# Performance work log

Hardware: AMD Instinct MI355X
Metric: run time of the kernel (lower is better)

Reference implementation:

```python
import jax, jax.numpy as jnp
import numpy as np

DIM_HEAD = 32  # from init_kwargs; scale = dim_head**-0.5 per the Triton kernel


def setup_inputs() -> dict:
    key = jax.random.key(0)
    k1, k2 = jax.random.split(key)
    B, N, dim = 16, 8192, 128
    D = 4 * DIM_HEAD  # heads * dim_head
    x = jax.random.normal(k1, (B, N, dim), dtype=jnp.float32)
    # ParameterList of 16 stages, each Parameter is randn(2, dim, D) * 0.02
    qk_weights = jax.random.normal(k2, (16, 2, dim, D), dtype=jnp.float32) * 0.02
    return {"x": x, "qk_weights": qk_weights}


def reference(x, qk_weights):
    """FFT-inspired butterfly attention.

    At stage s (stride = 2**s), positions are grouped into blocks of 2*stride;
    the first `stride` elements of each block are 'a', the next `stride` are
    their butterfly partners 'b' (b = a + stride). Q/K are projected from the
    ORIGINAL x with per-stage weights; v is the running value buffer (init x).
    For each pair, a 2-way softmax over [qa.ka, qa.kb] mixes (va, vb).
    """
    B, N, dim = x.shape
    logN = int(round(np.log2(N)))
    D = qk_weights.shape[-1]
    scale = DIM_HEAD ** -0.5

    v = x
    for s in range(logN):
        stride = 1 << s
        Wq = qk_weights[s, 0]  # (dim, D)
        Wk = qk_weights[s, 1]
        q = jnp.einsum('bnd,de->bne', x, Wq) * scale  # (B,N,D)
        k = jnp.einsum('bnd,de->bne', x, Wk)
        G = N // (2 * stride)
        qr = q.reshape(B, G, 2, stride, D)
        kr = k.reshape(B, G, 2, stride, D)
        vr = v.reshape(B, G, 2, stride, dim)
        qa = qr[:, :, 0]
        ka, kb = kr[:, :, 0], kr[:, :, 1]
        va, vb = vr[:, :, 0], vr[:, :, 1]
        s_aa = jnp.sum(qa * ka, axis=-1)  # (B,G,stride)
        s_ab = jnp.sum(qa * kb, axis=-1)
        attn = jax.nn.softmax(jnp.stack([s_aa, s_ab], axis=-1), axis=-1)
        w0 = attn[..., 0:1]
        w1 = attn[..., 1:2]
        out_a = w0 * va + w1 * vb
        out_b = w1 * va + w0 * vb
        v = jnp.stack([out_a, out_b], axis=2).reshape(B, N, dim)
    return v
```

## Files before the change

### kernel.cpp

```cpp
#include <hip/hip_runtime.h>
#include <hip/hip_bf16.h>


typedef __bf16 bf16x8 __attribute__((ext_vector_type(8)));
typedef float  f32x4  __attribute__((ext_vector_type(4)));

#define XSTR 136
#define XB_BYTES  (128 * XSTR * 2)
#define PREP_LDS  (2 * XB_BYTES)
#define LDS_W2    XB_BYTES

#define XW 128
#define LDS_W4    (128 * XW * 2)

#define LDS_MIX   (128 * 128 * 4)

#define WS_DWT_OFF (512 * 1024)
#define DWT4_BYTES (13 * 1024 * 4 * 64 * 4)
#define WS_NEED4   (WS_DWT_OFF + DWT4_BYTES)

__device__ __forceinline__ float ubits(unsigned int u) {
    union { unsigned int u; float f; } v; v.u = u; return v.f;
}
__device__ __forceinline__ unsigned short f2bf(float f) {
    union { float f; unsigned int u; } v; v.f = f;
    unsigned int u = v.u;
    return (unsigned short)((u + 0x7fffu + ((u >> 16) & 1u)) >> 16);
}
__device__ __forceinline__ int swzr(int r) { return ((r >> 1) ^ (r >> 2)) & 15; }

#define DPP_MOV_F(x, ctrl) \
    __int_as_float(__builtin_amdgcn_update_dpp(0, __float_as_int(x), (ctrl), 0xF, 0xF, true))

__device__ __forceinline__ float xlane_u(float x, int u, int lane) {
    if (u == 0) return DPP_MOV_F(x, 0xB1);
    if (u == 1) return DPP_MOV_F(x, 0x4E);
    if (u == 2) return __int_as_float(__builtin_amdgcn_ds_swizzle(__float_as_int(x), 0x101F));
    if (u == 3) return __int_as_float(__builtin_amdgcn_ds_swizzle(__float_as_int(x), 0x201F));
    if (u == 4) return __int_as_float(__builtin_amdgcn_ds_swizzle(__float_as_int(x), 0x401F));
    return __int_as_float(__builtin_amdgcn_ds_bpermute((lane ^ 32) << 2, __float_as_int(x)));
}

__global__ __launch_bounds__(512)
void prep_kernel(const float* __restrict__ qkw, unsigned short* __restrict__ PT) {
    extern __shared__ char smem[];
    unsigned short* wkb = (unsigned short*)smem;
    unsigned short* wqb = (unsigned short*)(smem + XB_BYTES);
    const int s = blockIdx.x;
    const float* Wq = qkw + (size_t)s * 32768;
    const float* Wk = Wq + 16384;
    const int tid = threadIdx.x;
    const int rl = tid >> 5, c4 = tid & 31;
#pragma unroll
    for (int j = 0; j < 8; ++j) {
        int r = j * 16 + rl;
        float4 vq = ((const float4*)Wq)[r * 32 + c4];
        float4 vk = ((const float4*)Wk)[r * 32 + c4];
        ushort4 uq; uq.x = f2bf(vq.x); uq.y = f2bf(vq.y); uq.z = f2bf(vq.z); uq.w = f2bf(vq.w);
        ushort4 uk; uk.x = f2bf(vk.x); uk.y = f2bf(vk.y); uk.z = f2bf(vk.z); uk.w = f2bf(vk.w);
        *(ushort4*)(wqb + r * XSTR + c4 * 4) = uq;
        *(ushort4*)(wkb + r * XSTR + c4 * 4) = uk;
    }
    __syncthreads();
    const int lane = tid & 63, w = tid >> 6;
    const int lane15 = lane & 15, quad = lane >> 4;
    f32x4 acc[8] = {};
#pragma unroll
    for (int kk = 0; kk < 4; ++kk) {
        bf16x8 a = *(const bf16x8*)(wkb + (w * 16 + lane15) * XSTR + kk * 32 + quad * 8);
#pragma unroll
        for (int ct = 0; ct < 8; ++ct) {
            bf16x8 b = *(const bf16x8*)(wqb + (ct * 16 + lane15) * XSTR + kk * 32 + quad * 8);
            acc[ct] = __builtin_amdgcn_mfma_f32_16x16x32_bf16(a, b, acc[ct], 0, 0, 0);
        }
    }
    unsigned short* dst = PT + s * 16384;
#pragma unroll
    for (int ct = 0; ct < 8; ++ct) {
        const int kkf = ct >> 1;
        const int qf  = (ct & 1) * 2 + (lane15 >> 3);
        const int e   = lane15 & 7;
#pragma unroll
        for (int r = 0; r < 4; ++r) {
            int fi = (w * 4 + kkf) * 64 + qf * 16 + quad * 4 + r;
            dst[fi * 8 + e] = f2bf(acc[ct][r] * 0.17677669529663687f);
        }
    }
}

__device__ __forceinline__ void stage_xb(unsigned short* xb, const float* xsrc,
                                         int tid, int base, int h_off, int rstride) {
    const int rl = tid >> 5, c4 = tid & 31;
#pragma unroll
    for (int j = 0; j < 8; ++j) {
        int i  = j * 16 + rl;
        int gp = base + (i >> 6) * h_off + (i & 63) * rstride;
        float4 val = ((const float4*)xsrc)[gp * 32 + c4];
        ushort4 us; us.x = f2bf(val.x); us.y = f2bf(val.y);
        us.z = f2bf(val.z); us.w = f2bf(val.w);
        *(ushort4*)(xb + i * XSTR + c4 * 4) = us;
    }
}

__device__ __forceinline__ void stage_xb_swz(unsigned short* xb, const float* xsrc,
                                             int tid, int base, int h_off, int rstride) {
    const int rl = tid >> 5, c4 = tid & 31;
#pragma unroll
    for (int j = 0; j < 8; ++j) {
        int i  = j * 16 + rl;
        int gp = base + (i >> 6) * h_off + (i & 63) * rstride;
        float4 val = ((const float4*)xsrc)[gp * 32 + c4];
        ushort4 us; us.x = f2bf(val.x); us.y = f2bf(val.y);
        us.z = f2bf(val.z); us.w = f2bf(val.w);
        int slot = c4 >> 1, half = c4 & 1;
        *(ushort4*)(xb + i * XW + (((slot ^ swzr(i)) << 3) + half * 4)) = us;
    }
}

template<int NS>
__device__ __forceinline__ void weights_body(const float* __restrict__ xsrc,
                                             const unsigned short* __restrict__ PT,
                                             float* __restrict__ dwt,
                                             unsigned short* xb, int tid, int bid,
                                             int s0, int base_mul, int h_off, int rstride)
{
    const int b    = bid >> 6;
    const int sub  = bid & 63;
    const int base = b * 8192 + sub * base_mul;

    stage_xb_swz(xb, xsrc, tid, base, h_off, rstride);

    const int lane = tid & 63, w = tid >> 6;
    const int lane15 = lane & 15, quad = lane >> 4;
    const int dh = w >> 1;
    const int ph = w & 1;

    uint4 af[2][2][4];
    {
        const uint4* Pf = (const uint4*)PT + (size_t)s0 * 2048;
#pragma unroll
        for (int mt = 0; mt < 2; ++mt)
#pragma unroll
            for (int kk = 0; kk < 4; ++kk)
                af[0][mt][kk] = Pf[((dh * 2 + mt) * 4 + kk) * 64 + lane];
    }
    __syncthreads();

#pragma unroll
    for (int u = 0; u < NS; ++u) {
        const int cur = u & 1, nxt = cur ^ 1;
        const int t   = 1 << u;
        const int tm1 = t - 1;

        if (u + 1 < NS) {
            const uint4* Pf = (const uint4*)PT + (size_t)(s0 + u + 1) * 2048;
#pragma unroll
            for (int mt = 0; mt < 2; ++mt)
#pragma unroll
                for (int kk = 0; kk < 4; ++kk)
                    af[nxt][mt][kk] = Pf[((dh * 2 + mt) * 4 + kk) * 64 + lane];
        }

        f32x4 acc[2][2] = {};
#pragma unroll
        for (int pg = 0; pg < 2; ++pg) {
            const int p  = (ph * 2 + pg) * 16 + lane15;
            const int ar = ((p & ~tm1) << 1) | (p & tm1);
            const int swa = swzr(ar);
            const unsigned short* brow = xb + ar * XW;
#pragma unroll
            for (int kk = 0; kk < 4; ++kk) {
                bf16x8 bfrag = *(const bf16x8*)(brow + (((kk * 4 + quad) ^ swa) << 3));
#pragma unroll
                for (int mt = 0; mt < 2; ++mt) {
                    union { uint4 u; bf16x8 b; } av; av.u = af[cur][mt][kk];
                    acc[mt][pg] = __builtin_amdgcn_mfma_f32_16x16x32_bf16(av.b, bfrag, acc[mt][pg], 0, 0, 0);
                }
            }
        }

        float sm[2];
#pragma unroll
        for (int pg = 0; pg < 2; ++pg) {
            const int p  = (ph * 2 + pg) * 16 + lane15;
            const int ar = ((p & ~tm1) << 1) | (p & tm1);
            const int br = ar + t;
            const int swa = swzr(ar), swb = swzr(br);
            float s = 0.f;
#pragma unroll
            for (int mt = 0; mt < 2; ++mt) {
                const int slot = dh * 4 + mt * 2 + (quad >> 1);
                uint2 ua = *(const uint2*)(xb + ar * XW + (((slot ^ swa) << 3) + (quad & 1) * 4));
                uint2 ub = *(const uint2*)(xb + br * XW + (((slot ^ swb) << 3) + (quad & 1) * 4));
                float a0 = ubits(ua.x << 16), a1 = ubits(ua.x & 0xffff0000u);
                float a2 = ubits(ua.y << 16), a3 = ubits(ua.y & 0xffff0000u);
                float b0 = ubits(ub.x << 16), b1 = ubits(ub.x & 0xffff0000u);
                float b2 = ubits(ub.y << 16), b3 = ubits(ub.y & 0xffff0000u);
                s += acc[mt][pg][0] * (a0 - b0) + acc[mt][pg][1] * (a1 - b1)
                   + acc[mt][pg][2] * (a2 - b2) + acc[mt][pg][3] * (a3 - b3);
            }
            s += xlane_u(s, 4, lane);
            s += xlane_u(s, 5, lane);
            sm[pg] = s;
        }
        float v = (lane & 16) ? sm[1] : sm[0];
        if (lane < 32)
            dwt[(((size_t)(s0 + u) * 1024 + bid) * 4 + dh) * 64 + ph * 32 + (lane & 31)] = v;
    }
}

__global__ __launch_bounds__(512, 4)
void weights_all_kernel(const float* __restrict__ xsrc,
                        const unsigned short* __restrict__ PT,
                        float* __restrict__ dwt)
{
    extern __shared__ char smem[];
    unsigned short* xb = (unsigned short*)smem;
    const int tid = threadIdx.x;
    if (blockIdx.x < 1024) {
        weights_body<7>(xsrc, PT, dwt, xb, tid, blockIdx.x,
                        0, 128, 64, 1);
    } else {
        weights_body<6>(xsrc, PT, dwt, xb, tid, blockIdx.x - 1024,
                        7, 2, 1, 128);
    }
}

template<int NS>
__global__ __launch_bounds__(512, 4)
void weights2_kernel(const float* __restrict__ xsrc,
                     const unsigned short* __restrict__ PT,
                     float* __restrict__ dwt,
                     int s0, int base_mul, int h_off, int rstride)
{
    extern __shared__ char smem[];
    unsigned short* xb = (unsigned short*)smem;

    const int tid  = threadIdx.x;
    const int b    = blockIdx.x >> 6;
    const int sub  = blockIdx.x & 63;
    const int base = b * 8192 + sub * base_mul;

    stage_xb(xb, xsrc, tid, base, h_off, rstride);

    const int lane = tid & 63, w = tid >> 6;
    const int lane15 = lane & 15, quad = lane >> 4;
    const int nt = w & 3;
    const int mh = w >> 2;
    const int p  = nt * 16 + lane15;

    __syncthreads();

#pragma unroll
    for (int u = 0; u < NS; ++u) {
        const int t   = 1 << u;
        const int tm1 = t - 1;
        const int ar  = ((p & ~tm1) << 1) | (p & tm1);

        float sm = 0.f;
        {
            const uint4* Pf = (const uint4*)PT + (size_t)(s0 + u) * 2048;
            const unsigned short* brow = xb + ar * XSTR + quad * 8;
            f32x4 acc[4] = {};
#pragma unroll
            for (int kk = 0; kk < 4; ++kk) {
                bf16x8 bfrag = *(const bf16x8*)(brow + kk * 32);
#pragma unroll
                for (int mt = 0; mt < 4; ++mt) {
                    union { uint4 u; bf16x8 b; } av;
                    av.u = Pf[((mh * 4 + mt) * 4 + kk) * 64 + lane];
                    acc[mt] = __builtin_amdgcn_mfma_f32_16x16x32_bf16(av.b, bfrag, acc[mt], 0, 0, 0);
                }
            }
            const unsigned short* da = xb + ar * XSTR + mh * 64 + quad * 4;
            const unsigned short* db = da + t * XSTR;
#pragma unroll
            for (int mt = 0; mt < 4; ++mt) {
                uint2 ua = *(const uint2*)(da + mt * 16);
                uint2 ub = *(const uint2*)(db + mt * 16);
                float a0 = ubits(ua.x << 16), a1 = ubits(ua.x & 0xffff0000u);
                float a2 = ubits(ua.y << 16), a3 = ubits(ua.y & 0xffff0000u);
                float b0 = ubits(ub.x << 16), b1 = ubits(ub.x & 0xffff0000u);
                float b2 = ubits(ub.y << 16), b3 = ubits(ub.y & 0xffff0000u);
                sm += acc[mt][0] * (a0 - b0) + acc[mt][1] * (a1 - b1)
                    + acc[mt][2] * (a2 - b2) + acc[mt][3] * (a3 - b3);
            }
        }
        sm += xlane_u(sm, 4, lane);
        sm += xlane_u(sm, 5, lane);
        if (lane < 16)
            dwt[((size_t)(s0 + u) * 1024 + blockIdx.x) * 128 + mh * 64 + nt * 16 + lane] = sm;
    }
}

template<int NS, int NPART>
__global__ __launch_bounds__(512, 4)
void mix_kernel(const float* __restrict__ vsrc,
                float* __restrict__ vdst,
                const float* __restrict__ dwt,
                int s0, int base_mul, int h_off, int rstride)
{
    extern __shared__ char smem[];
    float* vbuf = (float*)smem;

    const int tid  = threadIdx.x;
    const int b    = blockIdx.x >> 6;
    const int sub  = blockIdx.x & 63;
    const int base = b * 8192 + sub * base_mul;
    const int lane = tid & 63, w = tid >> 6;
    const int rl = tid >> 5, c4 = tid & 31;

    float vlo[16], vhi[16];
    {
        int r0 = 2 * lane, r1 = r0 + 1;
        int gp0 = base + (r0 >> 6) * h_off + (r0 & 63) * rstride;
        int gp1 = base + (r1 >> 6) * h_off + (r1 & 63) * rstride;
        const float* p0 = vsrc + (size_t)gp0 * 128 + w * 16;
        const float* p1 = vsrc + (size_t)gp1 * 128 + w * 16;
#pragma unroll
        for (int j = 0; j < 4; ++j) {
            float4 a = ((const float4*)p0)[j];
            float4 c = ((const float4*)p1)[j];
            vlo[4*j] = a.x; vlo[4*j+1] = a.y; vlo[4*j+2] = a.z; vlo[4*j+3] = a.w;
            vhi[4*j] = c.x; vhi[4*j+1] = c.y; vhi[4*j+2] = c.z; vhi[4*j+3] = c.w;
        }
    }

#pragma unroll
    for (int u = 0; u < NS; ++u) {
        const float* dw = dwt + ((size_t)(s0 + u) * 1024 + blockIdx.x) * (NPART * 64);
        float d = 0.f;
#pragma unroll
        for (int k = 0; k < NPART; ++k) d += dw[k * 64 + lane];
        const float w0 = 1.0f / (1.0f + __expf(-d));
        if (u < NS - 1) {
            const bool isE = ((lane >> u) & 1) == 0;
            const float wk = isE ? w0 : 1.0f - w0;
#pragma unroll
            for (int j = 0; j < 16; ++j) {
                float a = vlo[j], c = vhi[j];
                float s    = a + c;
                float keep = c + wk * (a - c);
                float send = s - keep;
                float ex   = xlane_u(send, u, lane);
                vlo[j] = isE ? keep : ex;
                vhi[j] = isE ? ex : keep;
            }
        } else {
            const float w1 = 1.0f - w0;
#pragma unroll
            for (int j = 0; j < 16; ++j) {
                float a = vlo[j], c = vhi[j];
                float oa = w0 * a + w1 * c;
                vlo[j] = oa;
                vhi[j] = a + c - oa;
            }
        }
    }

    {
        const int FU = NS - 1;
        int r0 = ((lane >> FU) << (FU + 1)) | (lane & ((1 << FU) - 1));
        int r1 = r0 + (1 << FU);
#pragma unroll
        for (int j = 0; j < 4; ++j) {
            float4 a; a.x = vlo[4*j]; a.y = vlo[4*j+1]; a.z = vlo[4*j+2]; a.w = vlo[4*j+3];
            float4 c; c.x = vhi[4*j]; c.y = vhi[4*j+1]; c.z = vhi[4*j+2]; c.w = vhi[4*j+3];
            int slot = w * 4 + j;
            *(float4*)(vbuf + r0 * 128 + ((slot ^ (r0 & 31)) << 2)) = a;
            *(float4*)(vbuf + r1 * 128 + ((slot ^ (r1 & 31)) << 2)) = c;
        }
    }
    __syncthreads();

#pragma unroll
    for (int j = 0; j < 8; ++j) {
        int i  = j * 16 + rl;
        int gp = base + (i >> 6) * h_off + (i & 63) * rstride;
        ((float4*)vdst)[gp * 32 + c4] =
            *(const float4*)(vbuf + i * 128 + (((c4 ^ (i & 31)) << 2)));
    }
}

extern "C" void kernel_launch(void* const* d_in, const int* in_sizes, int n_in,
                              void* d_out, int out_size, void* d_ws, size_t ws_size,
                              hipStream_t stream) {
    const float* x   = (const float*)d_in[0];
    const float* qkw = (const float*)d_in[1];
    float* out = (float*)d_out;
    unsigned short* PT = (unsigned short*)d_ws;
    float* dwt = (float*)((char*)d_ws + WS_DWT_OFF);

    (void)hipFuncSetAttribute((const void*)prep_kernel,
                              hipFuncAttributeMaxDynamicSharedMemorySize, PREP_LDS);

    prep_kernel<<<13, 512, PREP_LDS, stream>>>(qkw, PT);

    if (ws_size >= (size_t)WS_NEED4) {
        (void)hipFuncSetAttribute((const void*)weights_all_kernel,
                                  hipFuncAttributeMaxDynamicSharedMemorySize, LDS_W4);
        (void)hipFuncSetAttribute((const void*)mix_kernel<7,4>,
                                  hipFuncAttributeMaxDynamicSharedMemorySize, LDS_MIX);
        (void)hipFuncSetAttribute((const void*)mix_kernel<6,4>,
                                  hipFuncAttributeMaxDynamicSharedMemorySize, LDS_MIX);

        weights_all_kernel<<<2048, 512, LDS_W4, stream>>>(x, PT, dwt);

        mix_kernel<7,4><<<1024, 512, LDS_MIX, stream>>>(
            x, out, dwt, 0, 128, 64, 1);
        mix_kernel<6,4><<<1024, 512, LDS_MIX, stream>>>(
            out, out, dwt, 7, 2, 1, 128);
    } else {
        (void)hipFuncSetAttribute((const void*)weights2_kernel<7>,
                                  hipFuncAttributeMaxDynamicSharedMemorySize, LDS_W2);
        (void)hipFuncSetAttribute((const void*)weights2_kernel<6>,
                                  hipFuncAttributeMaxDynamicSharedMemorySize, LDS_W2);
        (void)hipFuncSetAttribute((const void*)mix_kernel<7,2>,
                                  hipFuncAttributeMaxDynamicSharedMemorySize, LDS_MIX);
        (void)hipFuncSetAttribute((const void*)mix_kernel<6,2>,
                                  hipFuncAttributeMaxDynamicSharedMemorySize, LDS_MIX);

        weights2_kernel<7><<<1024, 512, LDS_W2, stream>>>(
            x, PT, dwt, 0, 128, 64, 1);
        mix_kernel<7,2><<<1024, 512, LDS_MIX, stream>>>(
            x, out, dwt, 0, 128, 64, 1);
        weights2_kernel<6><<<1024, 512, LDS_W2, stream>>>(
            x, PT, dwt, 7, 2, 1, 128);
        mix_kernel<6,2><<<1024, 512, LDS_MIX, stream>>>(
            out, out, dwt, 7, 2, 1, 128);
    }
}
```

Baseline: 197.3 us.

## Use packed bf16 convert, interleave weight blocks, hoist mix weight loads

Replaces the scalar software float-to-bf16 rounding with the hardware v_cvt_pk_bf16_f32 instruction when staging x and the weights into LDS. The combined weights kernel now alternates the two stage-group bodies across even and odd block indices, so the different workloads are spread over the grid instead of split into two halves. The mix kernel loads all per-stage logits up front, before the v loads, so those global reads are not serialized inside the butterfly loop. This adds register pressure in the mix kernel.

Result: no change. 199.3 us (+1.0%).

```diff
diff --git a/kernel.cpp b/kernel.cpp
--- a/kernel.cpp
+++ b/kernel.cpp
@@ -26,6 +26,11 @@
     union { float f; unsigned int u; } v; v.f = f;
     unsigned int u = v.u;
     return (unsigned short)((u + 0x7fffu + ((u >> 16) & 1u)) >> 16);
+}
+__device__ __forceinline__ unsigned int cvtpk(float lo, float hi) {
+    unsigned int r;
+    asm("v_cvt_pk_bf16_f32 %0, %1, %2" : "=v"(r) : "v"(lo), "v"(hi));
+    return r;
 }
 __device__ __forceinline__ int swzr(int r) { return ((r >> 1) ^ (r >> 2)) & 15; }
 
@@ -56,10 +61,10 @@
         int r = j * 16 + rl;
         float4 vq = ((const float4*)Wq)[r * 32 + c4];
         float4 vk = ((const float4*)Wk)[r * 32 + c4];
-        ushort4 uq; uq.x = f2bf(vq.x); uq.y = f2bf(vq.y); uq.z = f2bf(vq.z); uq.w = f2bf(vq.w);
-        ushort4 uk; uk.x = f2bf(vk.x); uk.y = f2bf(vk.y); uk.z = f2bf(vk.z); uk.w = f2bf(vk.w);
-        *(ushort4*)(wqb + r * XSTR + c4 * 4) = uq;
-        *(ushort4*)(wkb + r * XSTR + c4 * 4) = uk;
+        uint2 uq; uq.x = cvtpk(vq.x, vq.y); uq.y = cvtpk(vq.z, vq.w);
+        uint2 uk; uk.x = cvtpk(vk.x, vk.y); uk.y = cvtpk(vk.z, vk.w);
+        *(uint2*)(wqb + r * XSTR + c4 * 4) = uq;
+        *(uint2*)(wkb + r * XSTR + c4 * 4) = uk;
     }
     __syncthreads();
     const int lane = tid & 63, w = tid >> 6;
@@ -110,10 +115,9 @@
         int i  = j * 16 + rl;
         int gp = base + (i >> 6) * h_off + (i & 63) * rstride;
         float4 val = ((const float4*)xsrc)[gp * 32 + c4];
-        ushort4 us; us.x = f2bf(val.x); us.y = f2bf(val.y);
-        us.z = f2bf(val.z); us.w = f2bf(val.w);
+        uint2 us; us.x = cvtpk(val.x, val.y); us.y = cvtpk(val.z, val.w);
         int slot = c4 >> 1, half = c4 & 1;
-        *(ushort4*)(xb + i * XW + (((slot ^ swzr(i)) << 3) + half * 4)) = us;
+        *(uint2*)(xb + i * XW + (((slot ^ swzr(i)) << 3) + half * 4)) = us;
     }
 }
 
@@ -217,11 +221,12 @@
     extern __shared__ char smem[];
     unsigned short* xb = (unsigned short*)smem;
     const int tid = threadIdx.x;
-    if (blockIdx.x < 1024) {
-        weights_body<7>(xsrc, PT, dwt, xb, tid, blockIdx.x,
+    const int bid = blockIdx.x >> 1;
+    if ((blockIdx.x & 1) == 0) {
+        weights_body<7>(xsrc, PT, dwt, xb, tid, bid,
                         0, 128, 64, 1);
     } else {
-        weights_body<6>(xsrc, PT, dwt, xb, tid, blockIdx.x - 1024,
+        weights_body<6>(xsrc, PT, dwt, xb, tid, bid,
                         7, 2, 1, 128);
     }
 }
@@ -310,6 +315,16 @@
     const int lane = tid & 63, w = tid >> 6;
     const int rl = tid >> 5, c4 = tid & 31;
 
+    float dlt[NS];
+#pragma unroll
+    for (int u = 0; u < NS; ++u) {
+        const float* dw = dwt + ((size_t)(s0 + u) * 1024 + blockIdx.x) * (NPART * 64);
+        float d = 0.f;
+#pragma unroll
+        for (int k = 0; k < NPART; ++k) d += dw[k * 64 + lane];
+        dlt[u] = d;
+    }
+
     float vlo[16], vhi[16];
     {
         int r0 = 2 * lane, r1 = r0 + 1;
@@ -328,11 +343,7 @@
 
 #pragma unroll
     for (int u = 0; u < NS; ++u) {
-        const float* dw = dwt + ((size_t)(s0 + u) * 1024 + blockIdx.x) * (NPART * 64);
-        float d = 0.f;
-#pragma unroll
-        for (int k = 0; k < NPART; ++k) d += dw[k * 64 + lane];
-        const float w0 = 1.0f / (1.0f + __expf(-d));
+        const float w0 = 1.0f / (1.0f + __expf(-dlt[u]));
         if (u < NS - 1) {
             const bool isE = ((lane >> u) & 1) == 0;
             const float wk = isE ? w0 : 1.0f - w0;
```
